# Kernel tuning notes

Hardware: AMD Instinct MI355X
Metric: run time of the kernel (lower is better)

Reference implementation:

```python
import jax, jax.numpy as jnp
import numpy as np

DIM = 256
NUM_HEADS = 8
HEAD_DIM = DIM // NUM_HEADS


def setup_inputs() -> dict:
    key = jax.random.key(0)
    k_x, k_wq, k_bq, k_wp, k_bp = jax.random.split(key, 5)
    B, C, H, W = 2, DIM, 48, 48
    x = jax.random.normal(k_x, (B, C, H, W), dtype=jnp.float32)
    # 1x1 convs are pointwise matmuls: store weights as [out, in]
    w_qkv = jax.random.normal(k_wq, (3 * C, C), dtype=jnp.float32) * (1.0 / np.sqrt(C))
    b_qkv = jax.random.normal(k_bq, (3 * C,), dtype=jnp.float32) * 0.01
    w_proj = jax.random.normal(k_wp, (C, C), dtype=jnp.float32) * (1.0 / np.sqrt(C))
    b_proj = jax.random.normal(k_bp, (C,), dtype=jnp.float32) * 0.01
    return {"x": x, "w_qkv": w_qkv, "b_qkv": b_qkv, "w_proj": w_proj, "b_proj": b_proj}


def reference(x, w_qkv, b_qkv, w_proj, b_proj):
    B, C, H, W = x.shape
    N = H * W
    # qkv 1x1 conv -> pointwise channel matmul
    qkv = jnp.einsum('bchw,oc->bohw', x, w_qkv) + b_qkv[None, :, None, None]
    q, k, v = jnp.split(qkv, 3, axis=1)  # each [B, C, H, W]
    q = q.reshape(B, NUM_HEADS, HEAD_DIM, N)
    k = k.reshape(B, NUM_HEADS, HEAD_DIM, N)
    v = v.reshape(B, NUM_HEADS, HEAD_DIM, N)
    scale = 1.0 / (HEAD_DIM ** 0.5)
    attn = jnp.einsum('bhdn,bhdm->bhnm', q, k) * scale  # [B, H, N, N]
    attn = jax.nn.softmax(attn, axis=-1)
    out = jnp.einsum('bhnm,bhdm->bhdn', attn, v)  # [B, heads, head_dim, N]
    out = out.reshape(B, C, H, W)
    out = jnp.einsum('bchw,oc->bohw', out, w_proj) + b_proj[None, :, None, None]
    return out + x
```

## Files before the change

kernel.cpp:

```cpp
#include <hip/hip_runtime.h>
#include <math.h>

#define C_DIM 256
#define NH 8
#define HD 32
#define BATCH 2
#define NPIX 2304
#define TK 64
#define NGRP (NPIX / 16)
#define TPB 18

typedef __attribute__((ext_vector_type(8))) short bf16x8;
typedef __attribute__((ext_vector_type(4))) float f32x4;

#define OFF_XT  0u
#define OFF_Q   1179648u
#define OFF_K   2359296u
#define OFF_V   3538944u
#define OFF_OT  4718592u
#define OFF_WQ  5898240u
#define OFF_WP  6094848u
#define OFF_F32 6160384u

__device__ __forceinline__ unsigned short f2b(float f) {
    union { float f; unsigned int u; } c; c.f = f;
    unsigned int u = c.u + 0x7FFFu + ((c.u >> 16) & 1u);
    return (unsigned short)(u >> 16);
}
__device__ __forceinline__ unsigned int pk2(float lo, float hi) {
    union { float f; unsigned int u; } a, b;
    a.f = lo; b.f = hi;
    return __builtin_amdgcn_perm(b.u + 0x8000u, a.u + 0x8000u, 0x07060302u);
}

__global__ __launch_bounds__(256) void prep_xt(
        const float* __restrict__ x, unsigned short* __restrict__ xT)
{
    __shared__ unsigned short t_s[64][72];
    const int tid = threadIdx.x;
    const int n0 = blockIdx.x * 64, c0 = blockIdx.y * 64, b = blockIdx.z;
    const int nl = tid & 63, cq = tid >> 6;
    #pragma unroll
    for (int p = 0; p < 8; ++p) {
        const int c = p * 8 + cq * 2;
        const float f0 = x[((size_t)b * C_DIM + c0 + c) * NPIX + n0 + nl];
        const float f1 = x[((size_t)b * C_DIM + c0 + c + 1) * NPIX + n0 + nl];
        *(unsigned int*)&t_s[nl][c] = pk2(f0, f1);
    }
    __syncthreads();
    const int row = tid >> 2, jq = tid & 3;
    #pragma unroll
    for (int hh = 0; hh < 2; ++hh) {
        const int jl = jq * 2 + hh;
        const int jg = blockIdx.y * 8 + jl;
        const int ngrp = blockIdx.x * 4 + (row >> 4);
        unsigned short* dst = xT + (((size_t)b * NGRP + ngrp) * 32 + jg) * 128 + (row & 15) * 8;
        *(uint4*)dst = *(uint4*)&t_s[row][jl * 8];
    }
}

__global__ __launch_bounds__(256) void prep_w(
        const float* __restrict__ wqkv, const float* __restrict__ wproj,
        unsigned short* __restrict__ wq, unsigned short* __restrict__ wp)
{
    const int t = blockIdx.x * 256 + threadIdx.x;
    const float* src; unsigned short* dst;
    if (t < 24576) {
        const int m = t >> 5, j = t & 31;
        src = wqkv + ((size_t)m * C_DIM + j * 8);
        dst = wq + ((size_t)((m >> 4) * 32 + j) * 16 + (m & 15)) * 8;
    } else {
        const int t2 = t - 24576, m = t2 >> 5, j = t2 & 31;
        src = wproj + ((size_t)m * C_DIM + j * 8);
        dst = wp + ((size_t)((m >> 4) * 32 + j) * 16 + (m & 15)) * 8;
    }
    const float4 f0 = *(const float4*)src, f1 = *(const float4*)(src + 4);
    *(uint4*)dst = make_uint4(pk2(f0.x, f0.y), pk2(f0.z, f0.w),
                              pk2(f1.x, f1.y), pk2(f1.z, f1.w));
}

__global__ __launch_bounds__(256, 2) void qkv_gemm(
        const unsigned short* __restrict__ xT, const unsigned short* __restrict__ wq,
        const float* __restrict__ bias,
        unsigned short* __restrict__ Qg, unsigned short* __restrict__ Kg,
        unsigned short* __restrict__ Vg)
{
    __shared__ unsigned short eplds[4][2560];
    const int tid = threadIdx.x, wv = tid >> 6, lane = tid & 63;
    const int l15 = lane & 15, quad = lane >> 4;
    const int n0 = blockIdx.x * 256, my = blockIdx.y, b = blockIdx.z;
    const int nw = n0 + wv * 64;

    bf16x8 af[2][8];
    #pragma unroll
    for (int mt = 0; mt < 2; ++mt)
        #pragma unroll
        for (int kc = 0; kc < 8; ++kc)
            af[mt][kc] = *(const bf16x8*)(wq +
                ((size_t)((my * 2 + mt) * 32 + kc * 4 + quad) * 16 + l15) * 8);

    f32x4 acc[2][4];
    #pragma unroll
    for (int mt = 0; mt < 2; ++mt)
        #pragma unroll
        for (int s = 0; s < 4; ++s) acc[mt][s] = (f32x4){0.f, 0.f, 0.f, 0.f};

    #pragma unroll
    for (int sub = 0; sub < 4; ++sub) {
        const int ngrp = (nw + sub * 16) >> 4;
        const unsigned short* bp = xT + ((size_t)b * NGRP + ngrp) * 32 * 128;
        #pragma unroll
        for (int kc = 0; kc < 8; ++kc) {
            const bf16x8 bf = *(const bf16x8*)(bp + (size_t)(kc * 4 + quad) * 128 + l15 * 8);
            acc[0][sub] = __builtin_amdgcn_mfma_f32_16x16x32_bf16(af[0][kc], bf, acc[0][sub], 0, 0, 0);
            acc[1][sub] = __builtin_amdgcn_mfma_f32_16x16x32_bf16(af[1][kc], bf, acc[1][sub], 0, 0, 0);
        }
    }

    const int which = my >> 3;
    const int h = my & 7, bh = b * NH + h;
    float4 b4[2];
    b4[0] = *(const float4*)(bias + my * 32 + quad * 4);
    b4[1] = *(const float4*)(bias + my * 32 + 16 + quad * 4);
    unsigned short* wl = eplds[wv];

    if (which < 2) {
        const float sc = (which == 0) ? 0.17677669529663687f : 1.0f;
        #pragma unroll
        for (int mt = 0; mt < 2; ++mt)
            #pragma unroll
            for (int sub = 0; sub < 4; ++sub) {
                const float v0 = (acc[mt][sub][0] + b4[mt].x) * sc;
                const float v1 = (acc[mt][sub][1] + b4[mt].y) * sc;
                const float v2 = (acc[mt][sub][2] + b4[mt].z) * sc;
                const float v3 = (acc[mt][sub][3] + b4[mt].w) * sc;
                *(uint2*)&wl[(sub * 16 + l15) * 40 + mt * 16 + quad * 4] =
                    make_uint2(pk2(v0, v1), pk2(v2, v3));
            }
        unsigned short* dst = ((which == 0) ? Qg : Kg)
                            + ((size_t)bh * NPIX + nw + lane) * HD;
        #pragma unroll
        for (int i = 0; i < 4; ++i)
            *((uint4*)dst + i) = *(uint4*)&wl[lane * 40 + i * 8];
    } else {
        #pragma unroll
        for (int mt = 0; mt < 2; ++mt)
            #pragma unroll
            for (int sub = 0; sub < 4; ++sub) {
                wl[(mt * 16 + quad * 4 + 0) * 72 + sub * 16 + l15] = f2b(acc[mt][sub][0] + b4[mt].x);
                wl[(mt * 16 + quad * 4 + 1) * 72 + sub * 16 + l15] = f2b(acc[mt][sub][1] + b4[mt].y);
                wl[(mt * 16 + quad * 4 + 2) * 72 + sub * 16 + l15] = f2b(acc[mt][sub][2] + b4[mt].z);
                wl[(mt * 16 + quad * 4 + 3) * 72 + sub * 16 + l15] = f2b(acc[mt][sub][3] + b4[mt].w);
            }
        const int row = lane >> 1, seg = (lane & 1) * 32;
        unsigned short* dst = Vg + ((size_t)bh * HD + row) * NPIX + nw + seg;
        #pragma unroll
        for (int i = 0; i < 4; ++i)
            *((uint4*)dst + i) = *(uint4*)&wl[row * 72 + seg + i * 8];
    }
}

__global__ __launch_bounds__(256, 4) void attn_kernel(
        const unsigned short* __restrict__ Qg, const unsigned short* __restrict__ Kg,
        const unsigned short* __restrict__ Vg,
        float* __restrict__ OtP, float* __restrict__ lsumP)
{
    __shared__ unsigned short k_s[2][TK][40];
    __shared__ unsigned short v_s[2][HD][76];
    __shared__ unsigned short p_s[4][16][76];

    const int tid  = threadIdx.x;
    const int wv   = tid >> 6;
    const int lane = tid & 63;
    const int l15  = lane & 15;
    const int quad = lane >> 4;
    const int bh   = blockIdx.x;
    const int q0   = blockIdx.y * 64;
    const int sp   = blockIdx.z;
    const int t0   = sp * TPB;

    const unsigned short* Qh = Qg + (size_t)bh * NPIX * HD;
    const unsigned short* Kh = Kg + (size_t)bh * NPIX * HD;
    const unsigned short* Vh = Vg + (size_t)bh * HD * NPIX;

    const bf16x8 q_frag = *(const bf16x8*)(Qh + (size_t)(q0 + wv * 16 + l15) * HD + quad * 8);

    const int kr = tid >> 2, kc = (tid & 3) * 8;
    const int vd = tid >> 3, vc = (tid & 7) * 8;

    uint4 kreg = *(const uint4*)(Kh + (size_t)(t0 * TK + kr) * HD + kc);
    uint4 vreg = *(const uint4*)(Vh + (size_t)vd * NPIX + t0 * TK + vc);
    *(uint4*)&k_s[0][kr][kc] = kreg;
    *(uint4*)&v_s[0][vd][vc] = vreg;

    f32x4 o0 = {0.f, 0.f, 0.f, 0.f};
    f32x4 o1 = {0.f, 0.f, 0.f, 0.f};
    float lsum = 0.f;

    for (int t = 0; t < TPB; ++t) {
        const int cur = t & 1;
        if (t + 1 < TPB) {
            const int k0 = (t0 + t + 1) * TK;
            kreg = *(const uint4*)(Kh + (size_t)(k0 + kr) * HD + kc);
            vreg = *(const uint4*)(Vh + (size_t)vd * NPIX + k0 + vc);
        }
        __syncthreads();

        f32x4 s[4];
        #pragma unroll
        for (int kg = 0; kg < 4; ++kg) {
            const bf16x8 kf = *(const bf16x8*)&k_s[cur][kg * 16 + l15][quad * 8];
            s[kg] = __builtin_amdgcn_mfma_f32_16x16x32_bf16(kf, q_frag,
                        (f32x4){0.f, 0.f, 0.f, 0.f}, 0, 0, 0);
        }

        #pragma unroll
        for (int kg = 0; kg < 4; ++kg) {
            const float p0 = __expf(s[kg][0]);
            const float p1 = __expf(s[kg][1]);
            const float p2 = __expf(s[kg][2]);
            const float p3 = __expf(s[kg][3]);
            lsum += (p0 + p1) + (p2 + p3);
            *(uint2*)&p_s[wv][l15][kg * 16 + quad * 4] =
                make_uint2(pk2(p0, p1), pk2(p2, p3));
        }

        #pragma unroll
        for (int kc2 = 0; kc2 < 2; ++kc2) {
            const bf16x8 pf  = *(const bf16x8*)&p_s[wv][l15][kc2 * 32 + quad * 8];
            const bf16x8 vf0 = *(const bf16x8*)&v_s[cur][l15][kc2 * 32 + quad * 8];
            const bf16x8 vf1 = *(const bf16x8*)&v_s[cur][16 + l15][kc2 * 32 + quad * 8];
            o0 = __builtin_amdgcn_mfma_f32_16x16x32_bf16(vf0, pf, o0, 0, 0, 0);
            o1 = __builtin_amdgcn_mfma_f32_16x16x32_bf16(vf1, pf, o1, 0, 0, 0);
        }

        if (t + 1 < TPB) {
            *(uint4*)&k_s[cur ^ 1][kr][kc] = kreg;
            *(uint4*)&v_s[cur ^ 1][vd][vc] = vreg;
        }
    }

    lsum += __shfl_xor(lsum, 16, 64);
    lsum += __shfl_xor(lsum, 32, 64);

    __syncthreads();
    float* pp = (float*)&p_s[wv][0][0];
    #pragma unroll
    for (int r = 0; r < 4; ++r) {
        pp[l15 * 36 + quad * 4 + r]      = o0[r];
        pp[l15 * 36 + 16 + quad * 4 + r] = o1[r];
    }
    if (quad == 0)
        lsumP[((size_t)sp * 16 + bh) * NPIX + q0 + wv * 16 + l15] = lsum;
    __syncthreads();
    const int q = lane >> 2, off = (lane & 3) * 8;
    float* dst = OtP + (((size_t)sp * 16 + bh) * NPIX + q0 + wv * 16 + q) * 32 + off;
    *(float4*)dst       = *(float4*)&pp[q * 36 + off];
    *((float4*)dst + 1) = *(float4*)&pp[q * 36 + off + 4];
}

__global__ __launch_bounds__(256) void norm_kernel(
        const float* __restrict__ OtP, const float* __restrict__ lsumP,
        unsigned short* __restrict__ OtT)
{
    const int q = blockIdx.x * 256 + threadIdx.x;
    const int bh = blockIdx.y;
    const float* pa = OtP + ((size_t)bh * NPIX + q) * 32;
    const float* pb = OtP + ((size_t)(16 + bh) * NPIX + q) * 32;
    const float inv = 1.f / (lsumP[(size_t)bh * NPIX + q] +
                             lsumP[(size_t)(16 + bh) * NPIX + q]);
    const int b = bh >> 3, h = bh & 7;
    unsigned short* cell = OtT + (((size_t)b * NGRP + (q >> 4)) * 32 + h * 4) * 128
                         + (q & 15) * 8;
    #pragma unroll
    for (int jq = 0; jq < 4; ++jq) {
        const float4 a0 = *(const float4*)(pa + jq * 8);
        const float4 a1 = *(const float4*)(pa + jq * 8 + 4);
        const float4 b0 = *(const float4*)(pb + jq * 8);
        const float4 b1 = *(const float4*)(pb + jq * 8 + 4);
        const float o0 = (a0.x + b0.x) * inv, o1 = (a0.y + b0.y) * inv;
        const float o2 = (a0.z + b0.z) * inv, o3 = (a0.w + b0.w) * inv;
        const float o4 = (a1.x + b1.x) * inv, o5 = (a1.y + b1.y) * inv;
        const float o6 = (a1.z + b1.z) * inv, o7 = (a1.w + b1.w) * inv;
        *(uint4*)(cell + jq * 128) = make_uint4(pk2(o0, o1), pk2(o2, o3),
                                                pk2(o4, o5), pk2(o6, o7));
    }
}

__global__ __launch_bounds__(256) void proj_gemm(
        const unsigned short* __restrict__ OtT, const unsigned short* __restrict__ wp,
        const float* __restrict__ bias, const float* __restrict__ x,
        float* __restrict__ out)
{
    __shared__ float plds[4][576];
    const int tid = threadIdx.x, wv = tid >> 6, lane = tid & 63;
    const int l15 = lane & 15, quad = lane >> 4;
    const int n0 = blockIdx.x * 128, my = blockIdx.y, b = blockIdx.z;
    const int nw = n0 + wv * 32;

    bf16x8 af[8];
    #pragma unroll
    for (int kc = 0; kc < 8; ++kc)
        af[kc] = *(const bf16x8*)(wp + ((size_t)(my * 32 + kc * 4 + quad) * 16 + l15) * 8);

    f32x4 acc[2];
    acc[0] = (f32x4){0.f, 0.f, 0.f, 0.f};
    acc[1] = (f32x4){0.f, 0.f, 0.f, 0.f};

    #pragma unroll
    for (int sub = 0; sub < 2; ++sub) {
        const int ngrp = (nw + sub * 16) >> 4;
        const unsigned short* bp = OtT + ((size_t)b * NGRP + ngrp) * 32 * 128;
        #pragma unroll
        for (int kc = 0; kc < 8; ++kc) {
            const bf16x8 bf = *(const bf16x8*)(bp + (size_t)(kc * 4 + quad) * 128 + l15 * 8);
            acc[sub] = __builtin_amdgcn_mfma_f32_16x16x32_bf16(af[kc], bf, acc[sub], 0, 0, 0);
        }
    }

    float* wl = plds[wv];
    #pragma unroll
    for (int sub = 0; sub < 2; ++sub) {
        wl[(quad * 4 + 0) * 36 + sub * 16 + l15] = acc[sub][0];
        wl[(quad * 4 + 1) * 36 + sub * 16 + l15] = acc[sub][1];
        wl[(quad * 4 + 2) * 36 + sub * 16 + l15] = acc[sub][2];
        wl[(quad * 4 + 3) * 36 + sub * 16 + l15] = acc[sub][3];
    }
    const int m0 = my * 16;
    #pragma unroll
    for (int p = 0; p < 2; ++p) {
        const int row = p * 8 + (lane >> 3), cn = (lane & 7) * 4;
        const int c = m0 + row;
        const size_t idx = ((size_t)b * C_DIM + c) * NPIX + nw + cn;
        const f32x4 v = *(const f32x4*)&wl[row * 36 + cn];
        const f32x4 r = *(const f32x4*)(x + idx);
        const float bv = bias[c];
        f32x4 o;
        o[0] = v[0] + bv + r[0]; o[1] = v[1] + bv + r[1];
        o[2] = v[2] + bv + r[2]; o[3] = v[3] + bv + r[3];
        *(f32x4*)(out + idx) = o;
    }
}

extern "C" void kernel_launch(void* const* d_in, const int* in_sizes, int n_in,
                              void* d_out, int out_size, void* d_ws, size_t ws_size,
                              hipStream_t stream)
{
    const float* x      = (const float*)d_in[0];
    const float* w_qkv  = (const float*)d_in[1];
    const float* b_qkv  = (const float*)d_in[2];
    const float* w_proj = (const float*)d_in[3];
    const float* b_proj = (const float*)d_in[4];
    float* out = (float*)d_out;

    unsigned short* ws = (unsigned short*)d_ws;
    unsigned short* xT  = ws + OFF_XT;
    unsigned short* Qg  = ws + OFF_Q;
    unsigned short* Kg  = ws + OFF_K;
    unsigned short* Vg  = ws + OFF_V;
    unsigned short* OtT = ws + OFF_OT;
    unsigned short* wq  = ws + OFF_WQ;
    unsigned short* wp  = ws + OFF_WP;
    float* fws   = (float*)(ws + OFF_F32);
    float* OtP   = fws;
    float* lsumP = fws + 4718592;

    prep_xt<<<dim3(36, 4, 2), 256, 0, stream>>>(x, xT);
    prep_w<<<dim3(128), 256, 0, stream>>>(w_qkv, w_proj, wq, wp);
    qkv_gemm<<<dim3(9, 24, 2), 256, 0, stream>>>(xT, wq, b_qkv, Qg, Kg, Vg);
    attn_kernel<<<dim3(16, 36, 2), 256, 0, stream>>>(Qg, Kg, Vg, OtP, lsumP);
    norm_kernel<<<dim3(9, 16), 256, 0, stream>>>(OtP, lsumP, OtT);
    proj_gemm<<<dim3(18, 16, 2), 256, 0, stream>>>(OtT, wp, b_proj, x, out);
}
```

Before: 117.9 us.

## Fuse split-K normalization into projection GEMM and merge prep kernels

Removes the separate norm_kernel by having proj_gemm read both fp32 split partial outputs and row sums, normalize, and pack to bf16 on the fly as the MFMA B operand. Merges prep_xt and prep_w into one launch indexed by a flat block id. This cuts two kernel launches and the intermediate bf16 OtT round trip through memory. The cost is that each projection block (16 output-channel tiles per pixel tile) re-reads the fp32 partials, adding redundant global traffic and division work. It also adds a __syncthreads before the LDS readback.

```diff
diff --git a/kernel.cpp b/kernel.cpp
--- a/kernel.cpp
+++ b/kernel.cpp
@@ -4,10 +4,9 @@
 #define C_DIM 256
 #define NH 8
 #define HD 32
-#define BATCH 2
 #define NPIX 2304
+#define NGRP 144
 #define TK 64
-#define NGRP (NPIX / 16)
 #define TPB 18
 
 typedef __attribute__((ext_vector_type(8))) short bf16x8;
@@ -17,7 +16,6 @@
 #define OFF_Q   1179648u
 #define OFF_K   2359296u
 #define OFF_V   3538944u
-#define OFF_OT  4718592u
 #define OFF_WQ  5898240u
 #define OFF_WP  6094848u
 #define OFF_F32 6160384u
@@ -33,50 +31,51 @@
     return __builtin_amdgcn_perm(b.u + 0x8000u, a.u + 0x8000u, 0x07060302u);
 }
 
-__global__ __launch_bounds__(256) void prep_xt(
-        const float* __restrict__ x, unsigned short* __restrict__ xT)
+__global__ __launch_bounds__(256) void prep_all(
+        const float* __restrict__ x, const float* __restrict__ wqkv,
+        const float* __restrict__ wproj, unsigned short* __restrict__ wsp)
 {
     __shared__ unsigned short t_s[64][72];
     const int tid = threadIdx.x;
-    const int n0 = blockIdx.x * 64, c0 = blockIdx.y * 64, b = blockIdx.z;
-    const int nl = tid & 63, cq = tid >> 6;
-    #pragma unroll
-    for (int p = 0; p < 8; ++p) {
-        const int c = p * 8 + cq * 2;
-        const float f0 = x[((size_t)b * C_DIM + c0 + c) * NPIX + n0 + nl];
-        const float f1 = x[((size_t)b * C_DIM + c0 + c + 1) * NPIX + n0 + nl];
-        *(unsigned int*)&t_s[nl][c] = pk2(f0, f1);
-    }
-    __syncthreads();
-    const int row = tid >> 2, jq = tid & 3;
-    #pragma unroll
-    for (int hh = 0; hh < 2; ++hh) {
-        const int jl = jq * 2 + hh;
-        const int jg = blockIdx.y * 8 + jl;
-        const int ngrp = blockIdx.x * 4 + (row >> 4);
-        unsigned short* dst = xT + (((size_t)b * NGRP + ngrp) * 32 + jg) * 128 + (row & 15) * 8;
-        *(uint4*)dst = *(uint4*)&t_s[row][jl * 8];
-    }
-}
-
-__global__ __launch_bounds__(256) void prep_w(
-        const float* __restrict__ wqkv, const float* __restrict__ wproj,
-        unsigned short* __restrict__ wq, unsigned short* __restrict__ wp)
-{
-    const int t = blockIdx.x * 256 + threadIdx.x;
-    const float* src; unsigned short* dst;
-    if (t < 24576) {
-        const int m = t >> 5, j = t & 31;
-        src = wqkv + ((size_t)m * C_DIM + j * 8);
-        dst = wq + ((size_t)((m >> 4) * 32 + j) * 16 + (m & 15)) * 8;
+    const int u = blockIdx.x;
+    if (u < 288) {
+        const int n0 = (u % 36) * 64, cb = (u / 36) % 4, b = u / 144;
+        const int c0 = cb * 64;
+        const int nl = tid & 63, cq = tid >> 6;
+        #pragma unroll
+        for (int p = 0; p < 8; ++p) {
+            const int c = p * 8 + cq * 2;
+            const float f0 = x[((size_t)b * C_DIM + c0 + c) * NPIX + n0 + nl];
+            const float f1 = x[((size_t)b * C_DIM + c0 + c + 1) * NPIX + n0 + nl];
+            *(unsigned int*)&t_s[nl][c] = pk2(f0, f1);
+        }
+        __syncthreads();
+        unsigned short* xT = wsp + OFF_XT;
+        const int row = tid >> 2, jq = tid & 3;
+        #pragma unroll
+        for (int hh = 0; hh < 2; ++hh) {
+            const int jl = jq * 2 + hh;
+            const int jg = cb * 8 + jl;
+            const int ngrp = (u % 36) * 4 + (row >> 4);
+            unsigned short* dst = xT + (((size_t)b * NGRP + ngrp) * 32 + jg) * 128 + (row & 15) * 8;
+            *(uint4*)dst = *(uint4*)&t_s[row][jl * 8];
+        }
     } else {
-        const int t2 = t - 24576, m = t2 >> 5, j = t2 & 31;
-        src = wproj + ((size_t)m * C_DIM + j * 8);
-        dst = wp + ((size_t)((m >> 4) * 32 + j) * 16 + (m & 15)) * 8;
-    }
-    const float4 f0 = *(const float4*)src, f1 = *(const float4*)(src + 4);
-    *(uint4*)dst = make_uint4(pk2(f0.x, f0.y), pk2(f0.z, f0.w),
-                              pk2(f1.x, f1.y), pk2(f1.z, f1.w));
+        const int t = (u - 288) * 256 + tid;
+        const float* src; unsigned short* dst;
+        if (t < 24576) {
+            const int m = t >> 5, j = t & 31;
+            src = wqkv + ((size_t)m * C_DIM + j * 8);
+            dst = wsp + OFF_WQ + ((size_t)((m >> 4) * 32 + j) * 16 + (m & 15)) * 8;
+        } else {
+            const int t2 = t - 24576, m = t2 >> 5, j = t2 & 31;
+            src = wproj + ((size_t)m * C_DIM + j * 8);
+            dst = wsp + OFF_WP + ((size_t)((m >> 4) * 32 + j) * 16 + (m & 15)) * 8;
+        }
+        const float4 f0 = *(const float4*)src, f1 = *(const float4*)(src + 4);
+        *(uint4*)dst = make_uint4(pk2(f0.x, f0.y), pk2(f0.z, f0.w),
+                                  pk2(f1.x, f1.y), pk2(f1.z, f1.w));
+    }
 }
 
 __global__ __launch_bounds__(256, 2) void qkv_gemm(
@@ -259,36 +258,9 @@
     *((float4*)dst + 1) = *(float4*)&pp[q * 36 + off + 4];
 }
 
-__global__ __launch_bounds__(256) void norm_kernel(
+__global__ __launch_bounds__(256) void proj_gemm(
         const float* __restrict__ OtP, const float* __restrict__ lsumP,
-        unsigned short* __restrict__ OtT)
-{
-    const int q = blockIdx.x * 256 + threadIdx.x;
-    const int bh = blockIdx.y;
-    const float* pa = OtP + ((size_t)bh * NPIX + q) * 32;
-    const float* pb = OtP + ((size_t)(16 + bh) * NPIX + q) * 32;
-    const float inv = 1.f / (lsumP[(size_t)bh * NPIX + q] +
-                             lsumP[(size_t)(16 + bh) * NPIX + q]);
-    const int b = bh >> 3, h = bh & 7;
-    unsigned short* cell = OtT + (((size_t)b * NGRP + (q >> 4)) * 32 + h * 4) * 128
-                         + (q & 15) * 8;
-    #pragma unroll
-    for (int jq = 0; jq < 4; ++jq) {
-        const float4 a0 = *(const float4*)(pa + jq * 8);
-        const float4 a1 = *(const float4*)(pa + jq * 8 + 4);
-        const float4 b0 = *(const float4*)(pb + jq * 8);
-        const float4 b1 = *(const float4*)(pb + jq * 8 + 4);
-        const float o0 = (a0.x + b0.x) * inv, o1 = (a0.y + b0.y) * inv;
-        const float o2 = (a0.z + b0.z) * inv, o3 = (a0.w + b0.w) * inv;
-        const float o4 = (a1.x + b1.x) * inv, o5 = (a1.y + b1.y) * inv;
-        const float o6 = (a1.z + b1.z) * inv, o7 = (a1.w + b1.w) * inv;
-        *(uint4*)(cell + jq * 128) = make_uint4(pk2(o0, o1), pk2(o2, o3),
-                                                pk2(o4, o5), pk2(o6, o7));
-    }
-}
-
-__global__ __launch_bounds__(256) void proj_gemm(
-        const unsigned short* __restrict__ OtT, const unsigned short* __restrict__ wp,
+        const unsigned short* __restrict__ wp,
         const float* __restrict__ bias, const float* __restrict__ x,
         float* __restrict__ out)
 {
@@ -309,12 +281,23 @@
 
     #pragma unroll
     for (int sub = 0; sub < 2; ++sub) {
-        const int ngrp = (nw + sub * 16) >> 4;
-        const unsigned short* bp = OtT + ((size_t)b * NGRP + ngrp) * 32 * 128;
+        const int tq = nw + sub * 16 + l15;
         #pragma unroll
         for (int kc = 0; kc < 8; ++kc) {
-            const bf16x8 bf = *(const bf16x8*)(bp + (size_t)(kc * 4 + quad) * 128 + l15 * 8);
-            acc[sub] = __builtin_amdgcn_mfma_f32_16x16x32_bf16(af[kc], bf, acc[sub], 0, 0, 0);
+            const size_t rowA = ((size_t)b * NH + kc) * NPIX + tq;
+            const size_t rowB = ((size_t)(16 + b * NH + kc)) * NPIX + tq;
+            const float* pa = OtP + rowA * 32 + quad * 8;
+            const float* pb = OtP + rowB * 32 + quad * 8;
+            const float4 a0 = *(const float4*)pa, a1 = *(const float4*)(pa + 4);
+            const float4 c0 = *(const float4*)pb, c1 = *(const float4*)(pb + 4);
+            const float inv = 1.0f / (lsumP[rowA] + lsumP[rowB]);
+            union { uint4 u; bf16x8 v; } bfr;
+            bfr.u = make_uint4(
+                pk2((a0.x + c0.x) * inv, (a0.y + c0.y) * inv),
+                pk2((a0.z + c0.z) * inv, (a0.w + c0.w) * inv),
+                pk2((a1.x + c1.x) * inv, (a1.y + c1.y) * inv),
+                pk2((a1.z + c1.z) * inv, (a1.w + c1.w) * inv));
+            acc[sub] = __builtin_amdgcn_mfma_f32_16x16x32_bf16(af[kc], bfr.v, acc[sub], 0, 0, 0);
         }
     }
 
@@ -326,6 +309,7 @@
         wl[(quad * 4 + 2) * 36 + sub * 16 + l15] = acc[sub][2];
         wl[(quad * 4 + 3) * 36 + sub * 16 + l15] = acc[sub][3];
     }
+    __syncthreads();
     const int m0 = my * 16;
     #pragma unroll
     for (int p = 0; p < 2; ++p) {
@@ -358,17 +342,14 @@
     unsigned short* Qg  = ws + OFF_Q;
     unsigned short* Kg  = ws + OFF_K;
     unsigned short* Vg  = ws + OFF_V;
-    unsigned short* OtT = ws + OFF_OT;
     unsigned short* wq  = ws + OFF_WQ;
     unsigned short* wp  = ws + OFF_WP;
     float* fws   = (float*)(ws + OFF_F32);
     float* OtP   = fws;
     float* lsumP = fws + 4718592;
 
-    prep_xt<<<dim3(36, 4, 2), 256, 0, stream>>>(x, xT);
-    prep_w<<<dim3(128), 256, 0, stream>>>(w_qkv, w_proj, wq, wp);
+    prep_all<<<dim3(416), 256, 0, stream>>>(x, w_qkv, w_proj, ws);
     qkv_gemm<<<dim3(9, 24, 2), 256, 0, stream>>>(xT, wq, b_qkv, Qg, Kg, Vg);
     attn_kernel<<<dim3(16, 36, 2), 256, 0, stream>>>(Qg, Kg, Vg, OtP, lsumP);
-    norm_kernel<<<dim3(9, 16), 256, 0, stream>>>(OtP, lsumP, OtT);
-    proj_gemm<<<dim3(18, 16, 2), 256, 0, stream>>>(OtT, wp, b_proj, x, out);
-}
+    proj_gemm<<<dim3(18, 16, 2), 256, 0, stream>>>(OtP, lsumP, wp, b_proj, x, out);
+}
```

Result: slower. 129.3 us (+9.7%).
